# Optimization experiments

Measured on AMD Instinct MI355X. Metric: run time of the kernel, lower is better.

The kernel has to match this reference:

```python
import math
import jax, jax.numpy as jnp
import numpy as np

D_MODEL = 1024
NHEAD = 16
HEAD_DIM = D_MODEL // NHEAD
BATCH = 2
SEQ = 2048


def setup_inputs() -> dict:
    key = jax.random.key(0)
    ks = jax.random.split(key, 8)
    data = jax.random.normal(ks[0], (BATCH, SEQ, D_MODEL), dtype=jnp.float32)
    temporal = jax.random.uniform(ks[1], (BATCH, SEQ), dtype=jnp.float32)
    mask = jnp.zeros((SEQ, SEQ), dtype=jnp.float32)
    s = 1.0 / math.sqrt(D_MODEL)
    Wq = jax.random.normal(ks[2], (D_MODEL, D_MODEL), dtype=jnp.float32) * s
    Wk = jax.random.normal(ks[3], (D_MODEL, D_MODEL), dtype=jnp.float32) * s
    Wv = jax.random.normal(ks[4], (D_MODEL, D_MODEL), dtype=jnp.float32) * s
    bq = jax.random.normal(ks[5], (D_MODEL,), dtype=jnp.float32) * 0.02
    bk = jax.random.normal(ks[6], (D_MODEL,), dtype=jnp.float32) * 0.02
    bv = jax.random.normal(ks[7], (D_MODEL,), dtype=jnp.float32) * 0.02
    return {"data": data, "temporal": temporal, "mask": mask,
            "Wq": Wq, "bq": bq, "Wk": Wk, "bk": bk, "Wv": Wv, "bv": bv}


def _rotate_half_pairs(x):
    # x: [..., s] with s even; pairs (x0,x1) -> (-x1, x0) interleaved
    x2 = x.reshape(x.shape[:-1] + (-1, 2))  # [..., s//2, 2]
    rot = jnp.stack([-x2[..., 1], x2[..., 0]], axis=-1)
    return rot.reshape(x.shape)


def reference(data, temporal, mask, Wq, bq, Wk, bk, Wv, bv):
    B, L, D = data.shape
    H, S = NHEAD, HEAD_DIM
    scale = math.sqrt(S)

    query = (data @ Wq + bq).reshape(B, L, H, S)
    key_ = (data @ Wk + bk).reshape(B, L, H, S)
    value = (data @ Wv + bv).reshape(B, L, H, S)

    # freq = 10000^(-arange(0, S, 2)/S), repeat_interleave(2) -> [S]
    freq = jnp.power(10000.0, -jnp.arange(0, S, 2, dtype=jnp.float32) / S)
    freq = jnp.repeat(freq, 2)
    freqs = temporal[:, :, None] * freq[None, None, :]  # [B, L, S]
    cosine = jnp.cos(freqs)[:, :, None, :]  # [B, L, 1, S]
    sine = jnp.sin(freqs)[:, :, None, :]

    rq = query * cosine + _rotate_half_pairs(query) * sine
    rk = key_ * cosine + _rotate_half_pairs(key_) * sine

    logits = jnp.einsum('bqhs,bkhs->bhqk', rq, rk) / scale
    logits = logits + mask  # mask: [L, L], broadcasts over b,h
    weights = jax.nn.softmax(logits, axis=-1)
    context = jnp.einsum('bhqk,bkhs->bqhs', weights, value)
    return context.reshape(B, L, D)
```

## Files before the change

kernel.cpp:

```cpp
#include <hip/hip_runtime.h>
#include <hip/hip_bf16.h>

#define D_MODEL 1024
#define NHEAD   16
#define HEAD_DIM 64
#define BATCH   2
#define SEQ     2048
#define NTOK    (BATCH*SEQ)

#define FREQ_LOG2 0.20762050593046015f

typedef short  bfrag __attribute__((ext_vector_type(8)));
typedef float  ffrag __attribute__((ext_vector_type(4)));

__device__ inline ushort f2bf(float x) {
    __hip_bfloat16 h = __float2bfloat16(x);
    return __builtin_bit_cast(ushort, h);
}
__device__ inline void split_bf(float x, ushort& hi, ushort& lo) {
    __hip_bfloat16 h = __float2bfloat16(x);
    hi = __builtin_bit_cast(ushort, h);
    lo = f2bf(x - __bfloat162float(h));
}

__device__ inline void gload16(const ushort* g, ushort* l) {
    __builtin_amdgcn_global_load_lds(
        (const __attribute__((address_space(1))) void*)g,
        (__attribute__((address_space(3))) void*)l, 16, 0, 0);
}

__global__ __launch_bounds__(256)
void split_data(const float* __restrict__ x, ushort* __restrict__ hi,
                ushort* __restrict__ lo)
{
    const int i4 = (blockIdx.x * 256 + threadIdx.x) * 4;
    const float4 v = *(const float4*)(x + i4);
    ushort4 h, l;
    split_bf(v.x, h.x, l.x); split_bf(v.y, h.y, l.y);
    split_bf(v.z, h.z, l.z); split_bf(v.w, h.w, l.w);
    *(ushort4*)(hi + i4) = h;
    *(ushort4*)(lo + i4) = l;
}

__global__ __launch_bounds__(256)
void split_tr_w(const float* __restrict__ Wq, const float* __restrict__ Wk,
                const float* __restrict__ Wv, ushort* __restrict__ hi)
{
    const int z = blockIdx.z;
    const float* W = (z == 0) ? Wq : (z == 1) ? Wk : Wv;
    ushort* thi = hi + (size_t)z * D_MODEL * D_MODEL;

    __shared__ float T[64][65];
    const int t  = threadIdx.x;
    const int k0 = blockIdx.x * 64, n0 = blockIdx.y * 64;

    #pragma unroll
    for (int i = 0; i < 4; i++) {
        const int f = i * 256 + t, r = f >> 4, c = (f & 15) * 4;
        const float4 v = *(const float4*)(W + (size_t)(k0 + r) * D_MODEL + n0 + c);
        T[r][c] = v.x; T[r][c + 1] = v.y; T[r][c + 2] = v.z; T[r][c + 3] = v.w;
    }
    __syncthreads();
    #pragma unroll
    for (int i = 0; i < 4; i++) {
        const int f = i * 256 + t, nr = f >> 4, kc = (f & 15) * 4;
        ushort4 h;
        h.x = f2bf(T[kc + 0][nr]);
        h.y = f2bf(T[kc + 1][nr]);
        h.z = f2bf(T[kc + 2][nr]);
        h.w = f2bf(T[kc + 3][nr]);
        const size_t o = (size_t)(n0 + nr) * D_MODEL + k0 + kc;
        *(ushort4*)(thi + o) = h;
    }
}

#define BK 32

union GemmSM {
    ushort st[2][3][128 * BK];
    float  c[64 * 132];
};

__global__ __launch_bounds__(256, 3)
void gemm_qkv(const ushort* __restrict__ Ahi, const ushort* __restrict__ Alo,
              const ushort* __restrict__ WThi,
              const float* __restrict__ bq, const float* __restrict__ bk,
              const float* __restrict__ bv, const float* __restrict__ temporal,
              ushort* __restrict__ Qhi, ushort* __restrict__ Qlo,
              ushort* __restrict__ Khi,
              ushort* __restrict__ VT)
{
    __shared__ GemmSM sm;
    const int z  = blockIdx.z;
    const int m0 = blockIdx.x * 128;
    const int n0 = blockIdx.y * 128;
    const float* bias = (z == 0) ? bq : (z == 1) ? bk : bv;
    const ushort* Bh = WThi + (size_t)z * D_MODEL * D_MODEL;

    const int t = threadIdx.x;
    const int w = t >> 6, lane = t & 63;
    const int lane15 = lane & 15, quad8 = (lane >> 4) * 8, quad = lane >> 4;
    const int wm = (w >> 1) * 64, wn = (w & 1) * 64;

    ffrag acc[4][4];
    #pragma unroll
    for (int i = 0; i < 4; i++)
        #pragma unroll
        for (int j = 0; j < 4; j++) acc[i][j] = (ffrag){0.f, 0.f, 0.f, 0.f};

    const int wr = w * 32;
    const int lr = lane >> 2;
    const int lc = (((lane & 3) ^ ((lane >> 3) & 3))) * 8;

    auto stage = [&](int bsel, int k0) {
        #pragma unroll
        for (int ch = 0; ch < 2; ch++) {
            const int rb = wr + ch * 16;
            const ushort* ga = Ahi + (size_t)(m0 + rb + lr) * D_MODEL + k0 + lc;
            const ushort* gl = Alo + (size_t)(m0 + rb + lr) * D_MODEL + k0 + lc;
            const ushort* gb = Bh  + (size_t)(n0 + rb + lr) * D_MODEL + k0 + lc;
            gload16(ga, &sm.st[bsel][0][rb * BK]);
            gload16(gl, &sm.st[bsel][1][rb * BK]);
            gload16(gb, &sm.st[bsel][2][rb * BK]);
        }
    };

    stage(0, 0);
    __syncthreads();

    const int rdsw = (quad ^ ((lane15 >> 1) & 3)) * 8;

    int buf = 0;
    for (int k0 = 0; k0 < D_MODEL; k0 += BK) {
        if (k0 + BK < D_MODEL) stage(buf ^ 1, k0 + BK);

        bfrag ah[4], al[4];
        #pragma unroll
        for (int mt = 0; mt < 4; mt++) {
            ah[mt] = *(const bfrag*)&sm.st[buf][0][(wm + mt * 16 + lane15) * BK + rdsw];
            al[mt] = *(const bfrag*)&sm.st[buf][1][(wm + mt * 16 + lane15) * BK + rdsw];
        }
        #pragma unroll
        for (int nt = 0; nt < 4; nt++) {
            const bfrag bh = *(const bfrag*)&sm.st[buf][2][(wn + nt * 16 + lane15) * BK + rdsw];
            #pragma unroll
            for (int mt = 0; mt < 4; mt++) {
                ffrag a = acc[mt][nt];
                a = __builtin_amdgcn_mfma_f32_16x16x32_bf16(ah[mt], bh, a, 0, 0, 0);
                a = __builtin_amdgcn_mfma_f32_16x16x32_bf16(al[mt], bh, a, 0, 0, 0);
                acc[mt][nt] = a;
            }
        }
        __syncthreads();
        buf ^= 1;
    }

    float bn[4];
    #pragma unroll
    for (int nt = 0; nt < 4; nt++) bn[nt] = bias[n0 + wn + nt * 16 + lane15];

    const int CST = (z == 2) ? 129 : 132;

    #pragma unroll
    for (int p = 0; p < 2; p++) {
        if (p) __syncthreads();
        if ((w >> 1) == p) {
            #pragma unroll
            for (int mt = 0; mt < 4; mt++)
                #pragma unroll
                for (int nt = 0; nt < 4; nt++)
                    #pragma unroll
                    for (int rr = 0; rr < 4; rr++)
                        sm.c[(mt * 16 + quad * 4 + rr) * CST + wn + nt * 16 + lane15] =
                            acc[mt][nt][rr] + bn[nt];
        }
        __syncthreads();

        if (z < 2) {
            ushort* ohi = (z == 0) ? Qhi : Khi;
            const float sc = (z == 0) ? 0.125f : 1.0f;
            #pragma unroll
            for (int i = 0; i < 8; i++) {
                const int f = i * 256 + t, r = f >> 5, c4 = (f & 31) * 4;
                float4 v = *(float4*)&sm.c[r * 132 + c4];
                const int m = m0 + p * 64 + r;
                const float tv = temporal[m];
                const float fr0 = exp2f(-(float)(c4 & 63) * FREQ_LOG2);
                const float fr1 = exp2f(-(float)((c4 + 2) & 63) * FREQ_LOG2);
                float s0, c0, s1, c1v;
                __sincosf(tv * fr0, &s0, &c0);
                __sincosf(tv * fr1, &s1, &c1v);
                const float y0 = (v.x * c0 - v.y * s0) * sc;
                const float y1 = (v.y * c0 + v.x * s0) * sc;
                const float y2 = (v.z * c1v - v.w * s1) * sc;
                const float y3 = (v.w * c1v + v.z * s1) * sc;
                ushort4 h, l;
                split_bf(y0, h.x, l.x); split_bf(y1, h.y, l.y);
                split_bf(y2, h.z, l.z); split_bf(y3, h.w, l.w);
                const size_t o = (size_t)m * D_MODEL + n0 + c4;
                *(ushort4*)(ohi + o) = h;
                if (z == 0) *(ushort4*)(Qlo + o) = l;
            }
        } else {
            const int bb = m0 >> 11;
            #pragma unroll
            for (int i = 0; i < 4; i++) {
                const int cid = i * 256 + t, col = cid >> 3, tg = (cid & 7) * 8;
                ushort u8[8];
                #pragma unroll
                for (int j = 0; j < 8; j++) u8[j] = f2bf(sm.c[(tg + j) * 129 + col]);
                const int ncol = n0 + col, hh = ncol >> 6, d = ncol & 63;
                const size_t dst = ((size_t)(bb * NHEAD + hh) * HEAD_DIM + d) * SEQ +
                                   (m0 & (SEQ - 1)) + p * 64 + tg;
                *(int4*)(VT + dst) = *(int4*)u8;
            }
        }
    }
}

__global__ __launch_bounds__(256, 4)
void attn_mfma(const ushort* __restrict__ Qhi, const ushort* __restrict__ Qlo,
               const ushort* __restrict__ Khi,
               const ushort* __restrict__ VT,  const float* __restrict__ mask,
               float* __restrict__ out)
{
    __shared__ ushort lsK[2][64 * 64], lsV[2][64 * 64], lsP[64 * 64];

    const int bid  = blockIdx.x;
    const int bh   = (bid & 7) * 4 + (bid >> 8);
    const int qb   = (bid >> 3) & 31;
    const int b    = bh >> 4, h = bh & 15;
    const int q0   = qb * 64;

    const int t = threadIdx.x, w = t >> 6, lane = t & 63;
    const int lane15 = lane & 15, quad = lane >> 4;
    const size_t tok0 = (size_t)b * SEQ;

    bfrag qh[2], ql[2];
    const size_t qrow = (tok0 + q0 + w * 16 + lane15) * D_MODEL + h * HEAD_DIM;
    #pragma unroll
    for (int ks = 0; ks < 2; ks++) {
        qh[ks] = *(const bfrag*)(Qhi + qrow + ks * 32 + quad * 8);
        ql[ks] = *(const bfrag*)(Qlo + qrow + ks * 32 + quad * 8);
    }

    ffrag of[4];
    #pragma unroll
    for (int nt = 0; nt < 4; nt++) of[nt] = (ffrag){0.f, 0.f, 0.f, 0.f};
    float l_i[4] = {0.f, 0.f, 0.f, 0.f};

    const int r1 = t >> 3,  c1 = (t & 7) * 8;
    const int sw = ((t & 7) ^ (r1 & 7)) * 8;
    const ushort* Kh0 = Khi + tok0 * D_MODEL + h * HEAD_DIM;
    const ushort* Vt0 = VT + (size_t)(b * NHEAD + h) * HEAD_DIM * SEQ;

    int4 pk0 = *(const int4*)(Kh0 + (size_t)r1 * D_MODEL + c1);
    int4 pk1 = *(const int4*)(Kh0 + (size_t)(32 + r1) * D_MODEL + c1);
    int4 pv0 = *(const int4*)(Vt0 + (size_t)r1 * SEQ + c1);
    int4 pv1 = *(const int4*)(Vt0 + (size_t)(32 + r1) * SEQ + c1);

    *(int4*)&lsK[0][r1 * 64 + sw]        = pk0;
    *(int4*)&lsK[0][(32 + r1) * 64 + sw] = pk1;
    *(int4*)&lsV[0][r1 * 64 + sw]        = pv0;
    *(int4*)&lsV[0][(32 + r1) * 64 + sw] = pv1;

    pk0 = *(const int4*)(Kh0 + (size_t)(64 + r1) * D_MODEL + c1);
    pk1 = *(const int4*)(Kh0 + (size_t)(96 + r1) * D_MODEL + c1);
    pv0 = *(const int4*)(Vt0 + (size_t)r1 * SEQ + 64 + c1);
    pv1 = *(const int4*)(Vt0 + (size_t)(32 + r1) * SEQ + 64 + c1);
    __syncthreads();

    const float* mrow = mask + (size_t)(q0 + w * 16 + quad * 4) * SEQ;

    const int krd = lane15 & 7;
    const int keyr = (((lane15 >> 2) & 3) << 1) | (lane15 & 1);

    int cur = 0;
    for (int kt = 0; kt < SEQ; kt += 64) {
        if (kt + 64 < SEQ) {
            *(int4*)&lsK[cur ^ 1][r1 * 64 + sw]        = pk0;
            *(int4*)&lsK[cur ^ 1][(32 + r1) * 64 + sw] = pk1;
            *(int4*)&lsV[cur ^ 1][r1 * 64 + sw]        = pv0;
            *(int4*)&lsV[cur ^ 1][(32 + r1) * 64 + sw] = pv1;
        }

        float mv[4][4];
        #pragma unroll
        for (int nt = 0; nt < 4; nt++)
            #pragma unroll
            for (int rr = 0; rr < 4; rr++)
                mv[nt][rr] = mrow[(size_t)rr * SEQ + kt + nt * 16 + lane15];

        const int ktn = (kt + 128 < SEQ) ? kt + 128 : 0;
        pk0 = *(const int4*)(Kh0 + (size_t)(ktn + r1) * D_MODEL + c1);
        pk1 = *(const int4*)(Kh0 + (size_t)(ktn + 32 + r1) * D_MODEL + c1);
        pv0 = *(const int4*)(Vt0 + (size_t)r1 * SEQ + ktn + c1);
        pv1 = *(const int4*)(Vt0 + (size_t)(32 + r1) * SEQ + ktn + c1);

        ffrag s[4];
        #pragma unroll
        for (int nt = 0; nt < 4; nt++) {
            ffrag a = (ffrag){0.f, 0.f, 0.f, 0.f};
            #pragma unroll
            for (int ks = 0; ks < 2; ks++) {
                const bfrag kf = *(const bfrag*)&lsK[cur][(nt * 16 + lane15) * 64 +
                                                          ((ks * 4 + quad) ^ krd) * 8];
                a = __builtin_amdgcn_mfma_f32_16x16x32_bf16(qh[ks], kf, a, 0, 0, 0);
                a = __builtin_amdgcn_mfma_f32_16x16x32_bf16(ql[ks], kf, a, 0, 0, 0);
            }
            s[nt] = a;
        }

        #pragma unroll
        for (int nt = 0; nt < 4; nt++) {
            #pragma unroll
            for (int rr = 0; rr < 4; rr++) {
                const float e = __expf(s[nt][rr] + mv[nt][rr]);
                l_i[rr] += e;
                const int prow = w * 16 + quad * 4 + rr;
                const int pchk = (2 * nt + (lane15 >> 3)) ^ ((quad << 1) | (rr & 1));
                lsP[prow * 64 + pchk * 8 + (lane15 & 7)] = f2bf(e);
            }
        }

        #pragma unroll
        for (int ks = 0; ks < 2; ks++) {
            const bfrag pf = *(const bfrag*)&lsP[(w * 16 + lane15) * 64 +
                                                 ((ks * 4 + quad) ^ keyr) * 8];
            #pragma unroll
            for (int nt = 0; nt < 4; nt++) {
                const bfrag vf = *(const bfrag*)&lsV[cur][(nt * 16 + lane15) * 64 +
                                                          ((ks * 4 + quad) ^ krd) * 8];
                of[nt] = __builtin_amdgcn_mfma_f32_16x16x32_bf16(pf, vf, of[nt], 0, 0, 0);
            }
        }

        __syncthreads();
        cur ^= 1;
    }

    float inv[4];
    #pragma unroll
    for (int rr = 0; rr < 4; rr++) {
        float v = l_i[rr];
        #pragma unroll
        for (int off = 1; off < 16; off <<= 1) v += __shfl_xor(v, off);
        inv[rr] = 1.0f / v;
    }
    #pragma unroll
    for (int nt = 0; nt < 4; nt++)
        #pragma unroll
        for (int rr = 0; rr < 4; rr++)
            out[(tok0 + q0 + w * 16 + quad * 4 + rr) * D_MODEL + h * HEAD_DIM +
                nt * 16 + lane15] = of[nt][rr] * inv[rr];
}

extern "C" void kernel_launch(void* const* d_in, const int* in_sizes, int n_in,
                              void* d_out, int out_size, void* d_ws, size_t ws_size,
                              hipStream_t stream)
{
    const float* data     = (const float*)d_in[0];
    const float* temporal = (const float*)d_in[1];
    const float* mask     = (const float*)d_in[2];
    const float* Wq = (const float*)d_in[3];
    const float* bq = (const float*)d_in[4];
    const float* Wk = (const float*)d_in[5];
    const float* bk = (const float*)d_in[6];
    const float* Wv = (const float*)d_in[7];
    const float* bv = (const float*)d_in[8];
    float* out = (float*)d_out;

    char* ws = (char*)d_ws;
    const size_t MB = 1024 * 1024;
    ushort* Ahi  = (ushort*)(ws + 0 * MB);
    ushort* Alo  = (ushort*)(ws + 8 * MB);
    ushort* WThi = (ushort*)(ws + 16 * MB);
    ushort* Qhi  = (ushort*)(ws + 28 * MB);
    ushort* Qlo  = (ushort*)(ws + 36 * MB);
    ushort* Khi  = (ushort*)(ws + 44 * MB);
    ushort* VT   = (ushort*)(ws + 60 * MB);

    split_data<<<dim3(NTOK * D_MODEL / 1024), 256, 0, stream>>>(data, Ahi, Alo);
    split_tr_w<<<dim3(16, 16, 3), 256, 0, stream>>>(Wq, Wk, Wv, WThi);
    gemm_qkv<<<dim3(NTOK / 128, D_MODEL / 128, 3), 256, 0, stream>>>(
        Ahi, Alo, WThi, bq, bk, bv, temporal,
        Qhi, Qlo, Khi, VT);
    attn_mfma<<<dim3(BATCH * NHEAD * SEQ / 64), 256, 0, stream>>>(
        Qhi, Qlo, Khi, VT, mask, out);
}
```

Baseline: 262.8 us.

## Process 128 query rows per attention block and convert mask to bf16

New measurement: 261.9 us. No clear change (-0.3%).

```diff
diff --git a/kernel.cpp b/kernel.cpp
--- a/kernel.cpp
+++ b/kernel.cpp
@@ -16,6 +16,9 @@
 __device__ inline ushort f2bf(float x) {
     __hip_bfloat16 h = __float2bfloat16(x);
     return __builtin_bit_cast(ushort, h);
+}
+__device__ inline float bf2f(ushort u) {
+    return __builtin_bit_cast(float, (uint)u << 16);
 }
 __device__ inline void split_bf(float x, ushort& hi, ushort& lo) {
     __hip_bfloat16 h = __float2bfloat16(x);
@@ -40,6 +43,16 @@
     split_bf(v.z, h.z, l.z); split_bf(v.w, h.w, l.w);
     *(ushort4*)(hi + i4) = h;
     *(ushort4*)(lo + i4) = l;
+}
+
+__global__ __launch_bounds__(256)
+void mask_bf(const float* __restrict__ m, ushort* __restrict__ o)
+{
+    const int i4 = (blockIdx.x * 256 + threadIdx.x) * 4;
+    const float4 v = *(const float4*)(m + i4);
+    ushort4 h;
+    h.x = f2bf(v.x); h.y = f2bf(v.y); h.z = f2bf(v.z); h.w = f2bf(v.w);
+    *(ushort4*)(o + i4) = h;
 }
 
 __global__ __launch_bounds__(256)
@@ -218,36 +231,45 @@
     }
 }
 
-__global__ __launch_bounds__(256, 4)
+__global__ __launch_bounds__(256, 2)
 void attn_mfma(const ushort* __restrict__ Qhi, const ushort* __restrict__ Qlo,
                const ushort* __restrict__ Khi,
-               const ushort* __restrict__ VT,  const float* __restrict__ mask,
+               const ushort* __restrict__ VT,  const ushort* __restrict__ maskbf,
                float* __restrict__ out)
 {
-    __shared__ ushort lsK[2][64 * 64], lsV[2][64 * 64], lsP[64 * 64];
+    __shared__ ushort lsK[2][64 * 64], lsV[2][64 * 64], lsP[128 * 64];
 
     const int bid  = blockIdx.x;
-    const int bh   = (bid & 7) * 4 + (bid >> 8);
-    const int qb   = (bid >> 3) & 31;
+    const int bh   = (bid & 7) * 4 + (bid >> 7);
+    const int qb   = (bid >> 3) & 15;
     const int b    = bh >> 4, h = bh & 15;
-    const int q0   = qb * 64;
+    const int q0   = qb * 128;
 
     const int t = threadIdx.x, w = t >> 6, lane = t & 63;
     const int lane15 = lane & 15, quad = lane >> 4;
     const size_t tok0 = (size_t)b * SEQ;
 
-    bfrag qh[2], ql[2];
-    const size_t qrow = (tok0 + q0 + w * 16 + lane15) * D_MODEL + h * HEAD_DIM;
-    #pragma unroll
-    for (int ks = 0; ks < 2; ks++) {
-        qh[ks] = *(const bfrag*)(Qhi + qrow + ks * 32 + quad * 8);
-        ql[ks] = *(const bfrag*)(Qlo + qrow + ks * 32 + quad * 8);
-    }
-
-    ffrag of[4];
-    #pragma unroll
-    for (int nt = 0; nt < 4; nt++) of[nt] = (ffrag){0.f, 0.f, 0.f, 0.f};
-    float l_i[4] = {0.f, 0.f, 0.f, 0.f};
+    bfrag qh[2][2], ql[2][2];
+    #pragma unroll
+    for (int su = 0; su < 2; su++) {
+        const size_t qrow = (tok0 + q0 + w * 32 + su * 16 + lane15) * D_MODEL +
+                            h * HEAD_DIM;
+        #pragma unroll
+        for (int ks = 0; ks < 2; ks++) {
+            qh[su][ks] = *(const bfrag*)(Qhi + qrow + ks * 32 + quad * 8);
+            ql[su][ks] = *(const bfrag*)(Qlo + qrow + ks * 32 + quad * 8);
+        }
+    }
+
+    ffrag of[2][4];
+    float l_i[2][4];
+    #pragma unroll
+    for (int su = 0; su < 2; su++)
+        #pragma unroll
+        for (int nt = 0; nt < 4; nt++) {
+            of[su][nt] = (ffrag){0.f, 0.f, 0.f, 0.f};
+            l_i[su][nt] = 0.f;
+        }
 
     const int r1 = t >> 3,  c1 = (t & 7) * 8;
     const int sw = ((t & 7) ^ (r1 & 7)) * 8;
@@ -270,9 +292,10 @@
     pv1 = *(const int4*)(Vt0 + (size_t)(32 + r1) * SEQ + 64 + c1);
     __syncthreads();
 
-    const float* mrow = mask + (size_t)(q0 + w * 16 + quad * 4) * SEQ;
-
-    const int krd = lane15 & 7;
+    const ushort* mrow0 = maskbf + (size_t)(q0 + w * 32 + quad * 4) * SEQ;
+    const ushort* mrow1 = maskbf + (size_t)(q0 + w * 32 + 16 + quad * 4) * SEQ;
+
+    const int krd  = lane15 & 7;
     const int keyr = (((lane15 >> 2) & 3) << 1) | (lane15 & 1);
 
     int cur = 0;
@@ -284,12 +307,14 @@
             *(int4*)&lsV[cur ^ 1][(32 + r1) * 64 + sw] = pv1;
         }
 
-        float mv[4][4];
+        float mv0[4][4], mv1[4][4];
         #pragma unroll
         for (int nt = 0; nt < 4; nt++)
             #pragma unroll
-            for (int rr = 0; rr < 4; rr++)
-                mv[nt][rr] = mrow[(size_t)rr * SEQ + kt + nt * 16 + lane15];
+            for (int rr = 0; rr < 4; rr++) {
+                mv0[nt][rr] = bf2f(mrow0[(size_t)rr * SEQ + kt + nt * 16 + lane15]);
+                mv1[nt][rr] = bf2f(mrow1[(size_t)rr * SEQ + kt + nt * 16 + lane15]);
+            }
 
         const int ktn = (kt + 128 < SEQ) ? kt + 128 : 0;
         pk0 = *(const int4*)(Kh0 + (size_t)(ktn + r1) * D_MODEL + c1);
@@ -297,41 +322,52 @@
         pv0 = *(const int4*)(Vt0 + (size_t)r1 * SEQ + ktn + c1);
         pv1 = *(const int4*)(Vt0 + (size_t)(32 + r1) * SEQ + ktn + c1);
 
-        ffrag s[4];
+        ffrag s0[4], s1[4];
         #pragma unroll
         for (int nt = 0; nt < 4; nt++) {
-            ffrag a = (ffrag){0.f, 0.f, 0.f, 0.f};
-            #pragma unroll
-            for (int ks = 0; ks < 2; ks++) {
-                const bfrag kf = *(const bfrag*)&lsK[cur][(nt * 16 + lane15) * 64 +
-                                                          ((ks * 4 + quad) ^ krd) * 8];
-                a = __builtin_amdgcn_mfma_f32_16x16x32_bf16(qh[ks], kf, a, 0, 0, 0);
-                a = __builtin_amdgcn_mfma_f32_16x16x32_bf16(ql[ks], kf, a, 0, 0, 0);
-            }
-            s[nt] = a;
-        }
-
-        #pragma unroll
-        for (int nt = 0; nt < 4; nt++) {
+            const bfrag kf0 = *(const bfrag*)&lsK[cur][(nt * 16 + lane15) * 64 +
+                                                       ((0 + quad) ^ krd) * 8];
+            const bfrag kf1 = *(const bfrag*)&lsK[cur][(nt * 16 + lane15) * 64 +
+                                                       ((4 + quad) ^ krd) * 8];
+            ffrag a0 = (ffrag){0.f, 0.f, 0.f, 0.f};
+            ffrag a1 = (ffrag){0.f, 0.f, 0.f, 0.f};
+            a0 = __builtin_amdgcn_mfma_f32_16x16x32_bf16(qh[0][0], kf0, a0, 0, 0, 0);
+            a0 = __builtin_amdgcn_mfma_f32_16x16x32_bf16(ql[0][0], kf0, a0, 0, 0, 0);
+            a0 = __builtin_amdgcn_mfma_f32_16x16x32_bf16(qh[0][1], kf1, a0, 0, 0, 0);
+            a0 = __builtin_amdgcn_mfma_f32_16x16x32_bf16(ql[0][1], kf1, a0, 0, 0, 0);
+            a1 = __builtin_amdgcn_mfma_f32_16x16x32_bf16(qh[1][0], kf0, a1, 0, 0, 0);
+            a1 = __builtin_amdgcn_mfma_f32_16x16x32_bf16(ql[1][0], kf0, a1, 0, 0, 0);
+            a1 = __builtin_amdgcn_mfma_f32_16x16x32_bf16(qh[1][1], kf1, a1, 0, 0, 0);
+            a1 = __builtin_amdgcn_mfma_f32_16x16x32_bf16(ql[1][1], kf1, a1, 0, 0, 0);
+            s0[nt] = a0;
+            s1[nt] = a1;
+        }
+
+        #pragma unroll
+        for (int nt = 0; nt < 4; nt++)
             #pragma unroll
             for (int rr = 0; rr < 4; rr++) {
-                const float e = __expf(s[nt][rr] + mv[nt][rr]);
-                l_i[rr] += e;
-                const int prow = w * 16 + quad * 4 + rr;
                 const int pchk = (2 * nt + (lane15 >> 3)) ^ ((quad << 1) | (rr & 1));
-                lsP[prow * 64 + pchk * 8 + (lane15 & 7)] = f2bf(e);
-            }
-        }
+                const float e0 = __expf(s0[nt][rr] + mv0[nt][rr]);
+                l_i[0][rr] += e0;
+                lsP[(w * 32 + quad * 4 + rr) * 64 + pchk * 8 + (lane15 & 7)] = f2bf(e0);
+                const float e1 = __expf(s1[nt][rr] + mv1[nt][rr]);
+                l_i[1][rr] += e1;
+                lsP[(w * 32 + 16 + quad * 4 + rr) * 64 + pchk * 8 + (lane15 & 7)] = f2bf(e1);
+            }
 
         #pragma unroll
         for (int ks = 0; ks < 2; ks++) {
-            const bfrag pf = *(const bfrag*)&lsP[(w * 16 + lane15) * 64 +
-                                                 ((ks * 4 + quad) ^ keyr) * 8];
+            const bfrag pf0 = *(const bfrag*)&lsP[(w * 32 + lane15) * 64 +
+                                                  ((ks * 4 + quad) ^ keyr) * 8];
+            const bfrag pf1 = *(const bfrag*)&lsP[(w * 32 + 16 + lane15) * 64 +
+                                                  ((ks * 4 + quad) ^ keyr) * 8];
             #pragma unroll
             for (int nt = 0; nt < 4; nt++) {
                 const bfrag vf = *(const bfrag*)&lsV[cur][(nt * 16 + lane15) * 64 +
                                                           ((ks * 4 + quad) ^ krd) * 8];
-                of[nt] = __builtin_amdgcn_mfma_f32_16x16x32_bf16(pf, vf, of[nt], 0, 0, 0);
+                of[0][nt] = __builtin_amdgcn_mfma_f32_16x16x32_bf16(pf0, vf, of[0][nt], 0, 0, 0);
+                of[1][nt] = __builtin_amdgcn_mfma_f32_16x16x32_bf16(pf1, vf, of[1][nt], 0, 0, 0);
             }
         }
 
@@ -339,20 +375,23 @@
         cur ^= 1;
     }
 
-    float inv[4];
-    #pragma unroll
-    for (int rr = 0; rr < 4; rr++) {
-        float v = l_i[rr];
-        #pragma unroll
-        for (int off = 1; off < 16; off <<= 1) v += __shfl_xor(v, off);
-        inv[rr] = 1.0f / v;
-    }
-    #pragma unroll
-    for (int nt = 0; nt < 4; nt++)
-        #pragma unroll
-        for (int rr = 0; rr < 4; rr++)
-            out[(tok0 + q0 + w * 16 + quad * 4 + rr) * D_MODEL + h * HEAD_DIM +
-                nt * 16 + lane15] = of[nt][rr] * inv[rr];
+    #pragma unroll
+    for (int su = 0; su < 2; su++) {
+        float inv[4];
+        #pragma unroll
+        for (int rr = 0; rr < 4; rr++) {
+            float v = l_i[su][rr];
+            #pragma unroll
+            for (int off = 1; off < 16; off <<= 1) v += __shfl_xor(v, off);
+            inv[rr] = 1.0f / v;
+        }
+        #pragma unroll
+        for (int nt = 0; nt < 4; nt++)
+            #pragma unroll
+            for (int rr = 0; rr < 4; rr++)
+                out[(tok0 + q0 + w * 32 + su * 16 + quad * 4 + rr) * D_MODEL +
+                    h * HEAD_DIM + nt * 16 + lane15] = of[su][nt][rr] * inv[rr];
+    }
 }
 
 extern "C" void kernel_launch(void* const* d_in, const int* in_sizes, int n_in,
@@ -379,12 +418,14 @@
     ushort* Qlo  = (ushort*)(ws + 36 * MB);
     ushort* Khi  = (ushort*)(ws + 44 * MB);
     ushort* VT   = (ushort*)(ws + 60 * MB);
+    ushort* Mbf  = (ushort*)(ws + 68 * MB);
 
     split_data<<<dim3(NTOK * D_MODEL / 1024), 256, 0, stream>>>(data, Ahi, Alo);
+    mask_bf<<<dim3(SEQ * SEQ / 1024), 256, 0, stream>>>(mask, Mbf);
     split_tr_w<<<dim3(16, 16, 3), 256, 0, stream>>>(Wq, Wk, Wv, WThi);
     gemm_qkv<<<dim3(NTOK / 128, D_MODEL / 128, 3), 256, 0, stream>>>(
         Ahi, Alo, WThi, bq, bk, bv, temporal,
         Qhi, Qlo, Khi, VT);
-    attn_mfma<<<dim3(BATCH * NHEAD * SEQ / 64), 256, 0, stream>>>(
-        Qhi, Qlo, Khi, VT, mask, out);
-}
+    attn_mfma<<<dim3(BATCH * NHEAD * SEQ / 128), 256, 0, stream>>>(
+        Qhi, Qlo, Khi, VT, Mbf, out);
+}
```
